# Kernel tuning notes

Hardware: AMD Instinct MI355X
Metric: run time of the kernel (lower is better)

## Reference

```python
import jax, jax.numpy as jnp
import numpy as np

IN_DIM = 256
HID = 256  # == n_qubits, required by c = f*c + i*g
SEQ = 512
BATCH = 256


def setup_inputs() -> dict:
    key = jax.random.key(0)
    ks = jax.random.split(key, 20)
    d = IN_DIM + HID
    lim = 1.0 / np.sqrt(d)
    inp = {
        "inputs": jax.random.normal(ks[0], (SEQ, BATCH, IN_DIM), dtype=jnp.float32),
        "h0": jnp.zeros((BATCH, HID), dtype=jnp.float32),
        "c0": jnp.zeros((BATCH, HID), dtype=jnp.float32),
    }
    names = ["f", "i", "u", "o"]
    for j, n in enumerate(names):
        inp["W" + n] = jax.random.uniform(ks[1 + 4 * j], (HID, d), jnp.float32, -lim, lim)
        inp["b" + n] = jax.random.uniform(ks[2 + 4 * j], (HID,), jnp.float32, -lim, lim)
        inp["theta" + n] = jax.random.normal(ks[3 + 4 * j], (HID,), dtype=jnp.float32)
        inp["scale" + n] = jax.random.uniform(ks[4 + 4 * j], (HID,), dtype=jnp.float32)
    return inp


def _qgate(z, theta, scale):
    # simulated quantum gate: sigmoid(sin(z * theta) * scale)
    return jax.nn.sigmoid(jnp.sin(z * theta) * scale)


def reference(inputs, h0, c0,
              Wf, bf, thetaf, scalef,
              Wi, bi, thetai, scalei,
              Wu, bu, thetau, scaleu,
              Wo, bo, thetao, scaleo):
    def step(carry, x):
        h, c = carry
        comb = jnp.concatenate([x, h], axis=1)  # [B, IN+HID]
        f = jax.nn.sigmoid(_qgate(comb @ Wf.T + bf, thetaf, scalef))
        i = jax.nn.sigmoid(_qgate(comb @ Wi.T + bi, thetai, scalei))
        g = jnp.tanh(_qgate(comb @ Wu.T + bu, thetau, scaleu))
        o = jax.nn.sigmoid(_qgate(comb @ Wo.T + bo, thetao, scaleo))
        c = f * c + i * g
        h = o * jnp.tanh(c)
        return (h, c), h

    (h_n, c_n), outputs = jax.lax.scan(step, (h0, c0), inputs)
    return outputs, (h_n, c_n)
```

## Files before the change

### kernel.cpp

```cpp
#include <hip/hip_runtime.h>
#include <cstdint>
#include <cstddef>


#define SEQ 512
#define BATCH 256
#define IN_DIMX 256
#define HIDN 256
#define DTOT 512

typedef float f32x4 __attribute__((ext_vector_type(4)));
typedef short s16x8 __attribute__((ext_vector_type(8)));

__device__ __forceinline__ unsigned short f2bf(float f) {
  unsigned u = __builtin_bit_cast(unsigned, f);
  u += 0x7FFFu + ((u >> 16) & 1u);
  return (unsigned short)(u >> 16);
}

__device__ __forceinline__ float sigm(float x) {
  return __builtin_amdgcn_rcpf(1.0f + __expf(-x));
}
__device__ __forceinline__ float tanh_fast(float x) {
  return 1.0f - 2.0f * __builtin_amdgcn_rcpf(1.0f + __expf(2.0f * x));
}

__global__ void qlstm_prep(const float* __restrict__ h0,
                           unsigned short* __restrict__ hbuf,
                           int* __restrict__ flags) {
  int tid = blockIdx.x * blockDim.x + threadIdx.x;
  if (tid < (SEQ + 2) * 4) flags[tid] = 0;
  int bm = tid >> 14, kc = (tid >> 9) & 31, row = (tid >> 3) & 63, j = tid & 7;
  hbuf[tid] = f2bf(h0[(bm * 64 + row) * HIDN + kc * 8 + j]);
}

__launch_bounds__(256, 1)
__global__ void qlstm_main(
    const float* __restrict__ X, const float* __restrict__ c0,
    const float* __restrict__ Wf, const float* __restrict__ bf_,
    const float* __restrict__ thf, const float* __restrict__ scf,
    const float* __restrict__ Wi, const float* __restrict__ bi_,
    const float* __restrict__ thi, const float* __restrict__ sci,
    const float* __restrict__ Wu, const float* __restrict__ bu_,
    const float* __restrict__ thu, const float* __restrict__ scu,
    const float* __restrict__ Wo, const float* __restrict__ bo_,
    const float* __restrict__ tho, const float* __restrict__ sco,
    float* __restrict__ out,
    unsigned short* __restrict__ hbuf,
    int* __restrict__ flags) {
  __shared__ __align__(16) unsigned short hA[32 * 64 * 8];

  const int tid = threadIdx.x;
  const int wave = tid >> 6;
  const int lane = tid & 63;
  const int quad = lane >> 4;
  const int col = lane & 15;
  const int bm = blockIdx.x & 3;
  const int js = blockIdx.x >> 2;

  s16x8 wx[4][8], wh[4][8];
  {
    const float* Wg[4] = {Wf, Wi, Wu, Wo};
#pragma unroll
    for (int g = 0; g < 4; ++g) {
      const float* wr = Wg[g] + (size_t)(js * 16 + col) * DTOT + quad * 8;
#pragma unroll
      for (int s = 0; s < 16; ++s) {
        float4 p0 = *(const float4*)(wr + s * 32);
        float4 p1 = *(const float4*)(wr + s * 32 + 4);
        s16x8 fr;
        fr[0] = (short)f2bf(p0.x); fr[1] = (short)f2bf(p0.y);
        fr[2] = (short)f2bf(p0.z); fr[3] = (short)f2bf(p0.w);
        fr[4] = (short)f2bf(p1.x); fr[5] = (short)f2bf(p1.y);
        fr[6] = (short)f2bf(p1.z); fr[7] = (short)f2bf(p1.w);
        if (s < 8) wx[g][s] = fr; else wh[g][s - 8] = fr;
      }
    }
  }
  float th[4], sc[4], bi[4];
  {
    const float* Tg[4] = {thf, thi, thu, tho};
    const float* Sg[4] = {scf, sci, scu, sco};
    const float* Bg[4] = {bf_, bi_, bu_, bo_};
#pragma unroll
    for (int g = 0; g < 4; ++g) {
      th[g] = Tg[g][js * 16 + col];
      sc[g] = Sg[g][js * 16 + col];
      bi[g] = Bg[g][js * 16 + col];
    }
  }

  const int browq = bm * 64 + wave * 16 + quad * 4;
  float c[4];
#pragma unroll
  for (int r = 0; r < 4; ++r)
    c[r] = c0[(size_t)(browq + r) * HIDN + js * 16 + col];

  const float* Xrow = X + (size_t)(bm * 64 + wave * 16 + col) * IN_DIMX + quad * 8;
  const int kc_out = js * 2 + (col >> 3);
  const int jsub = col & 7;

#pragma clang loop unroll(disable)
  for (int t = 0; t < SEQ; ++t) {
    float4 xv[8][2];
    {
      const float* xb = Xrow + (size_t)t * BATCH * IN_DIMX;
#pragma unroll
      for (int s = 0; s < 8; ++s) {
        xv[s][0] = *(const float4*)(xb + s * 32);
        xv[s][1] = *(const float4*)(xb + s * 32 + 4);
      }
    }
    if (t > 0) {
      if (tid == 0) {
        while (__hip_atomic_load(&flags[t * 4 + bm], __ATOMIC_ACQUIRE,
                                 __HIP_MEMORY_SCOPE_AGENT) < 16) {
          __builtin_amdgcn_s_sleep(2);
        }
      }
      __syncthreads();
    }
    {
      const unsigned short* hsrc = hbuf + ((size_t)((t & 1) * 4 + bm)) * 16384;
#pragma unroll
      for (int i = 0; i < 8; ++i) {
        int idx = i * 256 + tid;
        *(uint4*)&hA[idx * 8] = *(const uint4*)(hsrc + idx * 8);
      }
    }
    __syncthreads();

    s16x8 xf[8];
#pragma unroll
    for (int s = 0; s < 8; ++s) {
      s16x8 fr;
      fr[0] = (short)f2bf(xv[s][0].x); fr[1] = (short)f2bf(xv[s][0].y);
      fr[2] = (short)f2bf(xv[s][0].z); fr[3] = (short)f2bf(xv[s][0].w);
      fr[4] = (short)f2bf(xv[s][1].x); fr[5] = (short)f2bf(xv[s][1].y);
      fr[6] = (short)f2bf(xv[s][1].z); fr[7] = (short)f2bf(xv[s][1].w);
      xf[s] = fr;
    }

    f32x4 acc[4];
#pragma unroll
    for (int g = 0; g < 4; ++g) acc[g] = (f32x4){bi[g], bi[g], bi[g], bi[g]};

#pragma unroll
    for (int s = 0; s < 8; ++s) {
#pragma unroll
      for (int g = 0; g < 4; ++g)
        acc[g] = __builtin_amdgcn_mfma_f32_16x16x32_bf16(xf[s], wx[g][s], acc[g], 0, 0, 0);
    }
#pragma unroll
    for (int s = 0; s < 8; ++s) {
      s16x8 af = *(const s16x8*)&hA[((s * 4 + quad) * 64 + wave * 16 + col) * 8];
#pragma unroll
      for (int g = 0; g < 4; ++g)
        acc[g] = __builtin_amdgcn_mfma_f32_16x16x32_bf16(af, wh[g][s], acc[g], 0, 0, 0);
    }

    unsigned short* hdst = hbuf + ((size_t)(((t + 1) & 1) * 4 + bm)) * 16384;
    float* orow = out + (size_t)t * BATCH * HIDN;
#pragma unroll
    for (int r = 0; r < 4; ++r) {
      float fg = sigm(sigm(__sinf(acc[0][r] * th[0]) * sc[0]));
      float ig = sigm(sigm(__sinf(acc[1][r] * th[1]) * sc[1]));
      float gg = tanh_fast(sigm(__sinf(acc[2][r] * th[2]) * sc[2]));
      float og = sigm(sigm(__sinf(acc[3][r] * th[3]) * sc[3]));
      float cn = fg * c[r] + ig * gg;
      c[r] = cn;
      float hh = og * tanh_fast(cn);
      int brow = browq + r;
      orow[(size_t)brow * HIDN + js * 16 + col] = hh;
      hdst[(kc_out * 64 + (wave * 16 + quad * 4 + r)) * 8 + jsub] = f2bf(hh);
      if (t == SEQ - 1) {
        out[(size_t)SEQ * BATCH * HIDN + (size_t)brow * HIDN + js * 16 + col] = hh;
        out[(size_t)SEQ * BATCH * HIDN + (size_t)BATCH * HIDN +
            (size_t)brow * HIDN + js * 16 + col] = cn;
      }
    }
    __syncthreads();
    if (tid == 0)
      __hip_atomic_fetch_add(&flags[(t + 1) * 4 + bm], 1, __ATOMIC_RELEASE,
                             __HIP_MEMORY_SCOPE_AGENT);
  }
}

extern "C" void kernel_launch(void* const* d_in, const int* in_sizes, int n_in,
                              void* d_out, int out_size, void* d_ws, size_t ws_size,
                              hipStream_t stream) {
  (void)in_sizes; (void)n_in; (void)out_size; (void)ws_size;
  const float* X   = (const float*)d_in[0];
  const float* h0  = (const float*)d_in[1];
  const float* c0  = (const float*)d_in[2];
  const float* Wf  = (const float*)d_in[3];
  const float* bf_ = (const float*)d_in[4];
  const float* thf = (const float*)d_in[5];
  const float* scf = (const float*)d_in[6];
  const float* Wi  = (const float*)d_in[7];
  const float* bi_ = (const float*)d_in[8];
  const float* thi = (const float*)d_in[9];
  const float* sci = (const float*)d_in[10];
  const float* Wu  = (const float*)d_in[11];
  const float* bu_ = (const float*)d_in[12];
  const float* thu = (const float*)d_in[13];
  const float* scu = (const float*)d_in[14];
  const float* Wo  = (const float*)d_in[15];
  const float* bo_ = (const float*)d_in[16];
  const float* tho = (const float*)d_in[17];
  const float* sco = (const float*)d_in[18];
  float* out = (float*)d_out;

  unsigned short* hbuf = (unsigned short*)d_ws;
  int* flags = (int*)((char*)d_ws + 262144);

  hipLaunchKernelGGL(qlstm_prep, dim3(256), dim3(256), 0, stream, h0, hbuf, flags);

  hipLaunchKernelGGL(qlstm_main, dim3(64), dim3(256), 0, stream,
                     X, c0, Wf, bf_, thf, scf, Wi, bi_, thi, sci,
                     Wu, bu_, thu, scu, Wo, bo_, tho, sco,
                     out, hbuf, flags);
}
```

Before: 3.463 ms.

## Overlap input projection with flag wait and relax inter-block h exchange ordering

Moves the x-projection MFMAs ahead of the spin-wait on the per-step flag, so they can overlap with waiting for the other blocks. The new h is staged in LDS and written to the global exchange buffer as coalesced 64-bit relaxed atomic stores, and read back the same way with relaxed atomic loads. The acquire/release flag orderings are weakened to relaxed and the poll sleep is shortened, both to cut latency on the critical recurrent path. Output stores are deferred until after the flag signal. Relaxed ordering risks stale h reads across blocks, because no fence guarantees the data is visible before the flag.

After: 5.253 ms. 1.52x slower.

```diff
diff --git a/kernel.cpp b/kernel.cpp
--- a/kernel.cpp
+++ b/kernel.cpp
@@ -49,6 +49,7 @@
     unsigned short* __restrict__ hbuf,
     int* __restrict__ flags) {
   __shared__ __align__(16) unsigned short hA[32 * 64 * 8];
+  __shared__ __align__(16) unsigned short hS[2 * 64 * 8];
 
   const int tid = threadIdx.x;
   const int wave = tid >> 6;
@@ -97,60 +98,52 @@
     c[r] = c0[(size_t)(browq + r) * HIDN + js * 16 + col];
 
   const float* Xrow = X + (size_t)(bm * 64 + wave * 16 + col) * IN_DIMX + quad * 8;
-  const int kc_out = js * 2 + (col >> 3);
-  const int jsub = col & 7;
+  const int stage_off = ((col >> 3) * 64 + wave * 16 + quad * 4) * 8 + (col & 7);
 
 #pragma clang loop unroll(disable)
   for (int t = 0; t < SEQ; ++t) {
-    float4 xv[8][2];
+    f32x4 acc[4];
+#pragma unroll
+    for (int g = 0; g < 4; ++g) acc[g] = (f32x4){bi[g], bi[g], bi[g], bi[g]};
     {
       const float* xb = Xrow + (size_t)t * BATCH * IN_DIMX;
 #pragma unroll
       for (int s = 0; s < 8; ++s) {
-        xv[s][0] = *(const float4*)(xb + s * 32);
-        xv[s][1] = *(const float4*)(xb + s * 32 + 4);
-      }
-    }
+        float4 p0 = *(const float4*)(xb + s * 32);
+        float4 p1 = *(const float4*)(xb + s * 32 + 4);
+        s16x8 fr;
+        fr[0] = (short)f2bf(p0.x); fr[1] = (short)f2bf(p0.y);
+        fr[2] = (short)f2bf(p0.z); fr[3] = (short)f2bf(p0.w);
+        fr[4] = (short)f2bf(p1.x); fr[5] = (short)f2bf(p1.y);
+        fr[6] = (short)f2bf(p1.z); fr[7] = (short)f2bf(p1.w);
+#pragma unroll
+        for (int g = 0; g < 4; ++g)
+          acc[g] = __builtin_amdgcn_mfma_f32_16x16x32_bf16(fr, wx[g][s], acc[g], 0, 0, 0);
+      }
+    }
+
     if (t > 0) {
       if (tid == 0) {
-        while (__hip_atomic_load(&flags[t * 4 + bm], __ATOMIC_ACQUIRE,
+        while (__hip_atomic_load(&flags[t * 4 + bm], __ATOMIC_RELAXED,
                                  __HIP_MEMORY_SCOPE_AGENT) < 16) {
-          __builtin_amdgcn_s_sleep(2);
+          __builtin_amdgcn_s_sleep(1);
         }
       }
       __syncthreads();
     }
     {
-      const unsigned short* hsrc = hbuf + ((size_t)((t & 1) * 4 + bm)) * 16384;
-#pragma unroll
-      for (int i = 0; i < 8; ++i) {
+      const unsigned long long* hsrc =
+          (const unsigned long long*)(hbuf + ((size_t)((t & 1) * 4 + bm)) * 16384);
+      unsigned long long* dst = (unsigned long long*)hA;
+#pragma unroll
+      for (int i = 0; i < 16; ++i) {
         int idx = i * 256 + tid;
-        *(uint4*)&hA[idx * 8] = *(const uint4*)(hsrc + idx * 8);
+        dst[idx] = __hip_atomic_load(&hsrc[idx], __ATOMIC_RELAXED,
+                                     __HIP_MEMORY_SCOPE_AGENT);
       }
     }
     __syncthreads();
 
-    s16x8 xf[8];
-#pragma unroll
-    for (int s = 0; s < 8; ++s) {
-      s16x8 fr;
-      fr[0] = (short)f2bf(xv[s][0].x); fr[1] = (short)f2bf(xv[s][0].y);
-      fr[2] = (short)f2bf(xv[s][0].z); fr[3] = (short)f2bf(xv[s][0].w);
-      fr[4] = (short)f2bf(xv[s][1].x); fr[5] = (short)f2bf(xv[s][1].y);
-      fr[6] = (short)f2bf(xv[s][1].z); fr[7] = (short)f2bf(xv[s][1].w);
-      xf[s] = fr;
-    }
-
-    f32x4 acc[4];
-#pragma unroll
-    for (int g = 0; g < 4; ++g) acc[g] = (f32x4){bi[g], bi[g], bi[g], bi[g]};
-
-#pragma unroll
-    for (int s = 0; s < 8; ++s) {
-#pragma unroll
-      for (int g = 0; g < 4; ++g)
-        acc[g] = __builtin_amdgcn_mfma_f32_16x16x32_bf16(xf[s], wx[g][s], acc[g], 0, 0, 0);
-    }
 #pragma unroll
     for (int s = 0; s < 8; ++s) {
       s16x8 af = *(const s16x8*)&hA[((s * 4 + quad) * 64 + wave * 16 + col) * 8];
@@ -159,8 +152,7 @@
         acc[g] = __builtin_amdgcn_mfma_f32_16x16x32_bf16(af, wh[g][s], acc[g], 0, 0, 0);
     }
 
-    unsigned short* hdst = hbuf + ((size_t)(((t + 1) & 1) * 4 + bm)) * 16384;
-    float* orow = out + (size_t)t * BATCH * HIDN;
+    float hhr[4];
 #pragma unroll
     for (int r = 0; r < 4; ++r) {
       float fg = sigm(sigm(__sinf(acc[0][r] * th[0]) * sc[0]));
@@ -170,19 +162,36 @@
       float cn = fg * c[r] + ig * gg;
       c[r] = cn;
       float hh = og * tanh_fast(cn);
-      int brow = browq + r;
-      orow[(size_t)brow * HIDN + js * 16 + col] = hh;
-      hdst[(kc_out * 64 + (wave * 16 + quad * 4 + r)) * 8 + jsub] = f2bf(hh);
-      if (t == SEQ - 1) {
-        out[(size_t)SEQ * BATCH * HIDN + (size_t)brow * HIDN + js * 16 + col] = hh;
-        out[(size_t)SEQ * BATCH * HIDN + (size_t)BATCH * HIDN +
-            (size_t)brow * HIDN + js * 16 + col] = cn;
-      }
+      hhr[r] = hh;
+      hS[stage_off + r * 8] = f2bf(hh);
+    }
+    __syncthreads();
+
+    {
+      unsigned long long* hdst =
+          (unsigned long long*)(hbuf + ((size_t)(((t + 1) & 1) * 4 + bm)) * 16384) +
+          js * 256 + tid;
+      unsigned long long v = ((const unsigned long long*)hS)[tid];
+      __hip_atomic_store(hdst, v, __ATOMIC_RELAXED, __HIP_MEMORY_SCOPE_AGENT);
     }
     __syncthreads();
     if (tid == 0)
-      __hip_atomic_fetch_add(&flags[(t + 1) * 4 + bm], 1, __ATOMIC_RELEASE,
+      __hip_atomic_fetch_add(&flags[(t + 1) * 4 + bm], 1, __ATOMIC_RELAXED,
                              __HIP_MEMORY_SCOPE_AGENT);
+
+    {
+      float* orow = out + (size_t)t * BATCH * HIDN;
+#pragma unroll
+      for (int r = 0; r < 4; ++r) {
+        int brow = browq + r;
+        orow[(size_t)brow * HIDN + js * 16 + col] = hhr[r];
+        if (t == SEQ - 1) {
+          out[(size_t)SEQ * BATCH * HIDN + (size_t)brow * HIDN + js * 16 + col] = hhr[r];
+          out[(size_t)SEQ * BATCH * HIDN + (size_t)BATCH * HIDN +
+              (size_t)brow * HIDN + js * 16 + col] = c[r];
+        }
+      }
+    }
   }
 }
 
```
